# Kernel tuning notes

Measured on AMD Instinct MI355X. Metric: run time of the kernel, lower is better.

Reference implementation:

```python
import jax, jax.numpy as jnp
import numpy as np

B, C, H, W = 16, 256, 64, 64
K, HID, ITERS, EPS = 4, 512, 3, 1e-8


def _ln(x, g, b, eps=1e-5):
    m = jnp.mean(x, axis=-1, keepdims=True)
    v = jnp.mean((x - m) ** 2, axis=-1, keepdims=True)
    return (x - m) * jax.lax.rsqrt(v + eps) * g + b


def setup_inputs() -> dict:
    key = jax.random.key(0)
    ks = jax.random.split(key, 24)

    def lin(k, o, i):
        lim = np.sqrt(6.0 / (o + i)).astype(np.float32)
        return jax.random.uniform(k, (o, i), jnp.float32, -lim, lim)

    return {
        "x": jax.random.normal(ks[0], (B, C, H, W), jnp.float32),
        "noise": jax.random.normal(ks[1], (B, K, C), jnp.float32),
        "slot_mu": jax.random.normal(ks[2], (1, 1, C), jnp.float32),
        "slot_log_sigma": jnp.zeros((1, 1, C), jnp.float32),
        "ln_in_g": jnp.ones((C,)), "ln_in_b": jnp.zeros((C,)),
        "ln_sl_g": jnp.ones((C,)), "ln_sl_b": jnp.zeros((C,)),
        "ln_mlp_g": jnp.ones((C,)), "ln_mlp_b": jnp.zeros((C,)),
        "Wq": lin(ks[3], C, C), "bq": jnp.zeros((C,)),
        "Wk": lin(ks[4], C, C), "bk": jnp.zeros((C,)),
        "Wv": lin(ks[5], C, C), "bv": jnp.zeros((C,)),
        "Wu": lin(ks[6], C, 2 * C), "bu": jnp.zeros((C,)),
        "W1": lin(ks[7], HID, C), "b1": jnp.zeros((HID,)),
        "W2": lin(ks[8], C, HID), "b2": jnp.zeros((C,)),
        "We1": lin(ks[9], C // 2, C), "be1": jnp.zeros((C // 2,)),
        "We2": lin(ks[10], 1, C // 2), "be2": jnp.zeros((1,)),
    }


def reference(x, noise, slot_mu, slot_log_sigma, ln_in_g, ln_in_b, ln_sl_g, ln_sl_b,
              ln_mlp_g, ln_mlp_b, Wq, bq, Wk, bk, Wv, bv, Wu, bu, W1, b1, W2, b2,
              We1, be1, We2, be2):
    # b c h w -> b (h w) c
    xn = x.reshape(B, C, H * W).transpose(0, 2, 1)
    xn = _ln(xn, ln_in_g, ln_in_b)
    # k, v depend only on xn; hoisted out of the loop (same math)
    k = jnp.einsum('bnc,dc->bnd', xn, Wk) + bk
    v = jnp.einsum('bnc,dc->bnd', xn, Wv) + bv
    scale = C ** (-0.5)
    slots = slot_mu + jnp.exp(slot_log_sigma) * noise
    for _ in range(ITERS):
        prev = slots
        s = _ln(slots, ln_sl_g, ln_sl_b)
        q = jnp.einsum('bkc,dc->bkd', s, Wq) + bq
        attn = jax.nn.softmax(jnp.einsum('bkc,bnc->bkn', q, k) * scale, axis=1)
        w = attn / (jnp.sum(attn, axis=-1, keepdims=True) + EPS)
        updates = jnp.einsum('bkn,bnc->bkc', w, v)
        combined = jnp.concatenate([prev, updates], axis=-1)  # (B,K,2C)
        slots = jnp.einsum('bkc,dc->bkd', combined, Wu) + bu + prev
        m = _ln(slots, ln_mlp_g, ln_mlp_b)
        h = jax.nn.gelu(jnp.einsum('bkc,hc->bkh', m, W1) + b1, approximate=False)
        slots = slots + jnp.einsum('bkh,ch->bkc', h, W2) + b2
    e = jax.nn.gelu(jnp.einsum('bkc,dc->bkd', slots, We1) + be1, approximate=False)
    slot_weights = jax.nn.sigmoid(jnp.einsum('bkd,od->bko', e, We2) + be2)[..., 0]
    return slots, slot_weights
```

## Files before the change

kernel.cpp:

```cpp
#include <hip/hip_runtime.h>
#include <math.h>

#define B_    16
#define C_    256
#define NPIX  4096
#define K_    4
#define HID_  512
#define ITERS_ 3
#define NROWS (B_*NPIX)

typedef __attribute__((ext_vector_type(8))) short bf16x8;
typedef __attribute__((ext_vector_type(4))) float f32x4;

__device__ __forceinline__ float gelu_f(float x) {
    return 0.5f * x * (1.0f + erff(x * 0.70710678118654752f));
}

__device__ __forceinline__ unsigned short f2bf(float x) {
    union { float f; unsigned u; } v; v.f = x;
    unsigned r = v.u + 0x7fffu + ((v.u >> 16) & 1u);
    return (unsigned short)(r >> 16);
}
__device__ __forceinline__ float bflo(unsigned u) {
    union { unsigned u; float f; } v; v.u = u << 16; return v.f;
}
__device__ __forceinline__ float bfhi(unsigned u) {
    union { unsigned u; float f; } v; v.u = u & 0xffff0000u; return v.f;
}
__device__ __forceinline__ float4 shfl_xor4(float4 v, int m) {
    v.x = __shfl_xor(v.x, m); v.y = __shfl_xor(v.y, m);
    v.z = __shfl_xor(v.z, m); v.w = __shfl_xor(v.w, m);
    return v;
}

__device__ __forceinline__ void async_load16(const void* g, void* l) {
    __builtin_amdgcn_global_load_lds(
        (const __attribute__((address_space(1))) unsigned int*)g,
        (__attribute__((address_space(3))) unsigned int*)l, 16, 0, 0);
}

__device__ __forceinline__ void block_reduce2(float v1, float v2, float* red1, float* red2,
                                              int tid, float& o1, float& o2) {
    red1[tid] = v1; red2[tid] = v2;
    __syncthreads();
    for (int s = 128; s > 0; s >>= 1) {
        if (tid < s) { red1[tid] += red1[tid + s]; red2[tid] += red2[tid + s]; }
        __syncthreads();
    }
    o1 = red1[0]; o2 = red2[0];
    __syncthreads();
}

__global__ void prep_kernel(const float* __restrict__ Wk, const float* __restrict__ Wv,
                            const float* __restrict__ Wq, const float* __restrict__ Wu,
                            const float* __restrict__ W1, const float* __restrict__ W2,
                            const float* __restrict__ We1,
                            unsigned short* __restrict__ Wtb, float* __restrict__ WqT,
                            float* __restrict__ WuT, float* __restrict__ W1T,
                            float* __restrict__ W2T, float* __restrict__ We1T) {
    int t = blockIdx.x * 256 + threadIdx.x;
    if (t < 131072) {
        int d = t >> 8, c = t & 255;
        float v = (d < 256) ? Wk[d * 256 + c] : Wv[(d - 256) * 256 + c];
        Wtb[t] = f2bf(v);
    } else if (t < 196608) {
        int i = t - 131072; int c = i >> 8, d = i & 255;
        WqT[i] = Wq[d * 256 + c];
    } else if (t < 327680) {
        int i = t - 196608; int c = i >> 8, d = i & 255;
        WuT[i] = Wu[d * 512 + c];
    } else if (t < 458752) {
        int i = t - 327680; int c = i >> 9, h = i & 511;
        W1T[i] = W1[h * 256 + c];
    } else if (t < 589824) {
        int i = t - 458752; int h = i >> 8, d = i & 255;
        W2T[i] = W2[d * 512 + h];
    } else if (t < 622592) {
        int i = t - 589824; int c = i >> 7, e = i & 127;
        We1T[i] = We1[e * 256 + c];
    }
}

__global__ __launch_bounds__(256) void xn_fused_kernel(
    const float* __restrict__ x, const float* __restrict__ g, const float* __restrict__ bta,
    unsigned short* __restrict__ xnb) {
    __shared__ float tile[256][65];
    __shared__ float sg[256], sb[256];
    __shared__ float red1[256], red2[256];
    __shared__ float smean[64], srstd[64];
    const int tid = threadIdx.x;
    const int nt = blockIdx.x << 6, b = blockIdx.y;

    sg[tid] = g[tid]; sb[tid] = bta[tid];
    #pragma unroll
    for (int r = 0; r < 64; ++r) {
        int idx = tid + (r << 8);
        int c_l = idx >> 6, n_l = idx & 63;
        tile[c_l][n_l] = x[(size_t)(b * C_ + c_l) * NPIX + nt + n_l];
    }
    __syncthreads();
    {
        int cq = tid >> 6, n_l = tid & 63;
        float s = 0.f, s2 = 0.f;
        #pragma unroll 8
        for (int c = cq * 64; c < cq * 64 + 64; ++c) {
            float v = tile[c][n_l];
            s += v; s2 += v * v;
        }
        red1[tid] = s; red2[tid] = s2;
    }
    __syncthreads();
    if (tid < 64) {
        float s  = red1[tid] + red1[tid + 64] + red1[tid + 128] + red1[tid + 192];
        float s2 = red2[tid] + red2[tid + 64] + red2[tid + 128] + red2[tid + 192];
        float m = s * (1.0f / C_);
        smean[tid] = m;
        srstd[tid] = rsqrtf(s2 * (1.0f / C_) - m * m + 1e-5f);
    }
    __syncthreads();
    #pragma unroll
    for (int r = 0; r < 32; ++r) {
        int idx = tid + (r << 8);
        int n_l = idx >> 7, cp = idx & 127;
        int c0 = cp << 1;
        float mn = smean[n_l], rs = srstd[n_l];
        float v0 = (tile[c0][n_l] - mn) * rs * sg[c0] + sb[c0];
        float v1 = (tile[c0 + 1][n_l] - mn) * rs * sg[c0 + 1] + sb[c0 + 1];
        ushort2 o; o.x = f2bf(v0); o.y = f2bf(v1);
        *reinterpret_cast<ushort2*>(&xnb[((size_t)(b * NPIX + nt + n_l)) * C_ + c0]) = o;
    }
}

__global__ __launch_bounds__(256) void kv_gemm_mfma(
    const unsigned short* __restrict__ xnb, const unsigned short* __restrict__ Wtb,
    const float* __restrict__ bk, const float* __restrict__ bv,
    unsigned short* __restrict__ kbuf, unsigned short* __restrict__ vbuf) {
    __shared__ __align__(16) short As[128 * 32];
    __shared__ __align__(16) short Bs[128 * 32];
    const int tid = threadIdx.x;
    const int wave = tid >> 6, lane = tid & 63;
    const int mtile = blockIdx.x << 7;
    const int ntile = blockIdx.y << 7;
    const int wr = wave >> 1, wc = wave & 1;

    f32x4 acc[4][4];
    #pragma unroll
    for (int i = 0; i < 4; ++i)
        #pragma unroll
        for (int j = 0; j < 4; ++j) acc[i][j] = (f32x4)0.f;

    const int lrow = lane >> 2;
    const int lk   = (lane & 3) << 3;

    for (int kc0 = 0; kc0 < C_; kc0 += 32) {
        #pragma unroll
        for (int j = 0; j < 2; ++j) {
            int row = (wave << 5) + (j << 4) + lrow;
            async_load16(&xnb[(size_t)(mtile + row) * C_ + kc0 + lk],
                         &As[(wave << 10) + (j << 9)]);
            async_load16(&Wtb[(size_t)(ntile + row) * C_ + kc0 + lk],
                         &Bs[(wave << 10) + (j << 9)]);
        }
        __syncthreads();
        bf16x8 af[4], bfr[4];
        #pragma unroll
        for (int mi = 0; mi < 4; ++mi)
            af[mi] = *reinterpret_cast<const bf16x8*>(
                &As[((wr << 6) + (mi << 4) + (lane & 15)) * 32 + ((lane >> 4) << 3)]);
        #pragma unroll
        for (int ni = 0; ni < 4; ++ni)
            bfr[ni] = *reinterpret_cast<const bf16x8*>(
                &Bs[((wc << 6) + (ni << 4) + (lane & 15)) * 32 + ((lane >> 4) << 3)]);
        #pragma unroll
        for (int mi = 0; mi < 4; ++mi)
            #pragma unroll
            for (int ni = 0; ni < 4; ++ni)
                acc[mi][ni] = __builtin_amdgcn_mfma_f32_16x16x32_bf16(
                    af[mi], bfr[ni], acc[mi][ni], 0, 0, 0);
        __syncthreads();
    }

    #pragma unroll
    for (int ni = 0; ni < 4; ++ni) {
        int col = ntile + (wc << 6) + (ni << 4) + (lane & 15);
        bool is_k = (col < 256);
        float bias = is_k ? bk[col] : bv[col - 256];
        unsigned short* obuf = is_k ? kbuf : vbuf;
        int cl = is_k ? col : (col - 256);
        #pragma unroll
        for (int mi = 0; mi < 4; ++mi) {
            int row0 = mtile + (wr << 6) + (mi << 4) + ((lane >> 4) << 2);
            #pragma unroll
            for (int r = 0; r < 4; ++r)
                obuf[(size_t)(row0 + r) * C_ + cl] = f2bf(acc[mi][ni][r] + bias);
        }
    }
}

__device__ __forceinline__ void ln_q_body(float v, int tid, int r,
                                          const float* __restrict__ g_sl,
                                          const float* __restrict__ b_sl,
                                          const float* __restrict__ WqT,
                                          const float* __restrict__ bq,
                                          float* __restrict__ qbuf,
                                          float* snorm, float* red1, float* red2) {
    float sm, s2;
    block_reduce2(v, v * v, red1, red2, tid, sm, s2);
    float m = sm * (1.f / C_);
    float rs = rsqrtf(s2 * (1.f / C_) - m * m + 1e-5f);
    snorm[tid] = (v - m) * rs * g_sl[tid] + b_sl[tid];
    __syncthreads();
    float q0 = 0.f, q1 = 0.f, q2 = 0.f, q3 = 0.f;
    #pragma unroll 8
    for (int c = 0; c < C_; c += 4) {
        q0 = fmaf(WqT[(c + 0) * C_ + tid], snorm[c + 0], q0);
        q1 = fmaf(WqT[(c + 1) * C_ + tid], snorm[c + 1], q1);
        q2 = fmaf(WqT[(c + 2) * C_ + tid], snorm[c + 2], q2);
        q3 = fmaf(WqT[(c + 3) * C_ + tid], snorm[c + 3], q3);
    }
    qbuf[r * C_ + tid] = (q0 + q1) + (q2 + q3) + bq[tid];
}

__global__ __launch_bounds__(256) void slot_init_q_kernel(
    const float* __restrict__ noise, const float* __restrict__ mu,
    const float* __restrict__ log_sigma,
    const float* __restrict__ g_sl, const float* __restrict__ b_sl,
    const float* __restrict__ WqT, const float* __restrict__ bq,
    float* __restrict__ slots, float* __restrict__ qbuf) {
    __shared__ float snorm[256];
    __shared__ float red1[256], red2[256];
    int tid = threadIdx.x;
    int r = blockIdx.x;
    float v = mu[tid] + expf(log_sigma[tid]) * noise[r * C_ + tid];
    slots[r * C_ + tid] = v;
    ln_q_body(v, tid, r, g_sl, b_sl, WqT, bq, qbuf, snorm, red1, red2);
}

__global__ __launch_bounds__(256) void attn_fused_kernel(
    const float* __restrict__ qbuf, const unsigned short* __restrict__ kbuf,
    const unsigned short* __restrict__ vbuf,
    float* __restrict__ partials, float* __restrict__ asump) {
    __shared__ float4 qT[264];
    __shared__ float attns[K_][64];
    __shared__ float upd_s[K_][256];
    __shared__ float asw[4][4];

    const int tid = threadIdx.x;
    const int b = blockIdx.y;
    const int chunk = blockIdx.x;
    const int n0 = chunk << 6;
    const int wave = tid >> 6, lane = tid & 63;

    {
        int c = tid;
        float4 qv;
        qv.x = qbuf[b * 1024 + c];
        qv.y = qbuf[b * 1024 + 256 + c];
        qv.z = qbuf[b * 1024 + 512 + c];
        qv.w = qbuf[b * 1024 + 768 + c];
        qT[c + (c >> 5)] = qv;
    }
    __syncthreads();

    const int cpart = tid & 7;
    const int npair = tid >> 3;
    const int c0 = cpart << 5;
    float4 acc0 = {0.f, 0.f, 0.f, 0.f}, acc1 = {0.f, 0.f, 0.f, 0.f};
    const unsigned short* kbase = kbuf + ((size_t)b * NPIX + n0 + npair * 2) * C_ + c0;
    #pragma unroll
    for (int j = 0; j < 4; ++j) {
        uint4 k0 = *reinterpret_cast<const uint4*>(kbase + j * 8);
        uint4 k1 = *reinterpret_cast<const uint4*>(kbase + C_ + j * 8);
        const unsigned kw0[4] = {k0.x, k0.y, k0.z, k0.w};
        const unsigned kw1[4] = {k1.x, k1.y, k1.z, k1.w};
        #pragma unroll
        for (int jj = 0; jj < 4; ++jj) {
            int cidx = c0 + j * 8 + jj * 2 + cpart;
            float4 qa = qT[cidx];
            float4 qb = qT[cidx + 1];
            float f00 = bflo(kw0[jj]), f01 = bfhi(kw0[jj]);
            float f10 = bflo(kw1[jj]), f11 = bfhi(kw1[jj]);
            acc0.x += f00 * qa.x + f01 * qb.x;  acc0.y += f00 * qa.y + f01 * qb.y;
            acc0.z += f00 * qa.z + f01 * qb.z;  acc0.w += f00 * qa.w + f01 * qb.w;
            acc1.x += f10 * qa.x + f11 * qb.x;  acc1.y += f10 * qa.y + f11 * qb.y;
            acc1.z += f10 * qa.z + f11 * qb.z;  acc1.w += f10 * qa.w + f11 * qb.w;
        }
    }
    #pragma unroll
    for (int m = 1; m <= 4; m <<= 1) {
        acc0 = acc0 + shfl_xor4(acc0, m);
        acc1 = acc1 + shfl_xor4(acc1, m);
    }
    float4 w0, w1;
    {
        float4 l = acc0 * 0.0625f;
        float mx = fmaxf(fmaxf(l.x, l.y), fmaxf(l.z, l.w));
        w0.x = expf(l.x - mx); w0.y = expf(l.y - mx);
        w0.z = expf(l.z - mx); w0.w = expf(l.w - mx);
        float inv = 1.0f / (w0.x + w0.y + w0.z + w0.w);
        w0 = w0 * inv;
        l = acc1 * 0.0625f;
        mx = fmaxf(fmaxf(l.x, l.y), fmaxf(l.z, l.w));
        w1.x = expf(l.x - mx); w1.y = expf(l.y - mx);
        w1.z = expf(l.z - mx); w1.w = expf(l.w - mx);
        inv = 1.0f / (w1.x + w1.y + w1.z + w1.w);
        w1 = w1 * inv;
    }
    if (cpart == 0) {
        int n_l = npair * 2;
        attns[0][n_l] = w0.x; attns[1][n_l] = w0.y; attns[2][n_l] = w0.z; attns[3][n_l] = w0.w;
        attns[0][n_l + 1] = w1.x; attns[1][n_l + 1] = w1.y;
        attns[2][n_l + 1] = w1.z; attns[3][n_l + 1] = w1.w;
    }
    float4 ws = w0 + w1;
    #pragma unroll
    for (int m = 8; m <= 32; m <<= 1) ws = ws + shfl_xor4(ws, m);
    if (lane == 0) {
        asw[wave][0] = ws.x; asw[wave][1] = ws.y; asw[wave][2] = ws.z; asw[wave][3] = ws.w;
    }
    __syncthreads();
    if (tid < 4)
        asump[(b * 64 + chunk) * 4 + tid] =
            asw[0][tid] + asw[1][tid] + asw[2][tid] + asw[3][tid];

    const int h = wave >> 1;
    const int chalf = (wave & 1) << 7;
    const int c = chalf + lane * 2;
    float a0[K_] = {0.f, 0.f, 0.f, 0.f};
    float a1[K_] = {0.f, 0.f, 0.f, 0.f};
    const unsigned short* vbase = vbuf + ((size_t)b * NPIX + n0 + h * 32) * C_ + c;
    #pragma unroll 4
    for (int nn = 0; nn < 32; ++nn) {
        unsigned vv = *reinterpret_cast<const unsigned*>(vbase + (size_t)nn * C_);
        float v0 = bflo(vv), v1 = bfhi(vv);
        int n_l = h * 32 + nn;
        float q0 = attns[0][n_l], q1 = attns[1][n_l], q2 = attns[2][n_l], q3 = attns[3][n_l];
        a0[0] = fmaf(q0, v0, a0[0]); a1[0] = fmaf(q0, v1, a1[0]);
        a0[1] = fmaf(q1, v0, a0[1]); a1[1] = fmaf(q1, v1, a1[1]);
        a0[2] = fmaf(q2, v0, a0[2]); a1[2] = fmaf(q2, v1, a1[2]);
        a0[3] = fmaf(q3, v0, a0[3]); a1[3] = fmaf(q3, v1, a1[3]);
    }
    __syncthreads();
    if (h == 0) {
        #pragma unroll
        for (int k = 0; k < K_; ++k) { upd_s[k][c] = a0[k]; upd_s[k][c + 1] = a1[k]; }
    }
    __syncthreads();
    if (h == 1) {
        #pragma unroll
        for (int k = 0; k < K_; ++k) { upd_s[k][c] += a0[k]; upd_s[k][c + 1] += a1[k]; }
    }
    __syncthreads();
    float* pb = partials + (size_t)(b * 64 + chunk) * (K_ * 256);
    #pragma unroll
    for (int k = 0; k < K_; ++k) pb[k * 256 + tid] = upd_s[k][tid];
}

__device__ __forceinline__ float slot_update_body(
    int tid, int r, const float* __restrict__ slots,
    const float* __restrict__ partials, const float* __restrict__ asump,
    const float* __restrict__ WuT, const float* __restrict__ bu,
    const float* __restrict__ g_mlp, const float* __restrict__ b_mlp,
    const float* __restrict__ W1T, const float* __restrict__ b1,
    const float* __restrict__ W2T, const float* __restrict__ b2,
    float* comb, float* mrow, float* hrow, float* red1, float* red2) {
    int b = r >> 2, kk = r & 3;
    float prev = slots[r * C_ + tid];
    comb[tid] = prev;
    float u0 = 0.f, u1 = 0.f;
    #pragma unroll 8
    for (int j = 0; j < 64; j += 2) {
        u0 += partials[((size_t)(b * 64 + j) * 4 + kk) * 256 + tid];
        u1 += partials[((size_t)(b * 64 + j + 1) * 4 + kk) * 256 + tid];
    }
    float dv = (tid < 64) ? asump[(b * 64 + tid) * 4 + kk] : 0.f;
    float sm_d, dummy;
    block_reduce2(dv, 0.f, red1, red2, tid, sm_d, dummy);
    comb[256 + tid] = (u0 + u1) / (sm_d + 1e-8f);
    __syncthreads();
    float n0 = 0.f, n1 = 0.f, n2 = 0.f, n3 = 0.f;
    #pragma unroll 8
    for (int c = 0; c < 512; c += 4) {
        n0 = fmaf(WuT[(c + 0) * C_ + tid], comb[c + 0], n0);
        n1 = fmaf(WuT[(c + 1) * C_ + tid], comb[c + 1], n1);
        n2 = fmaf(WuT[(c + 2) * C_ + tid], comb[c + 2], n2);
        n3 = fmaf(WuT[(c + 3) * C_ + tid], comb[c + 3], n3);
    }
    float nv = (n0 + n1) + (n2 + n3) + bu[tid] + prev;
    float sm, s2;
    block_reduce2(nv, nv * nv, red1, red2, tid, sm, s2);
    float m = sm * (1.f / C_);
    float rs = rsqrtf(s2 * (1.f / C_) - m * m + 1e-5f);
    mrow[tid] = (nv - m) * rs * g_mlp[tid] + b_mlp[tid];
    __syncthreads();
    #pragma unroll
    for (int rep = 0; rep < 2; ++rep) {
        int j = tid + rep * 256;
        float h0 = 0.f, h1 = 0.f, h2 = 0.f, h3 = 0.f;
        #pragma unroll 8
        for (int c = 0; c < C_; c += 4) {
            h0 = fmaf(W1T[(c + 0) * HID_ + j], mrow[c + 0], h0);
            h1 = fmaf(W1T[(c + 1) * HID_ + j], mrow[c + 1], h1);
            h2 = fmaf(W1T[(c + 2) * HID_ + j], mrow[c + 2], h2);
            h3 = fmaf(W1T[(c + 3) * HID_ + j], mrow[c + 3], h3);
        }
        hrow[j] = gelu_f((h0 + h1) + (h2 + h3) + b1[j]);
    }
    __syncthreads();
    float o0 = 0.f, o1 = 0.f, o2 = 0.f, o3 = 0.f;
    #pragma unroll 8
    for (int h = 0; h < 512; h += 4) {
        o0 = fmaf(W2T[(h + 0) * C_ + tid], hrow[h + 0], o0);
        o1 = fmaf(W2T[(h + 1) * C_ + tid], hrow[h + 1], o1);
        o2 = fmaf(W2T[(h + 2) * C_ + tid], hrow[h + 2], o2);
        o3 = fmaf(W2T[(h + 3) * C_ + tid], hrow[h + 3], o3);
    }
    return nv + (o0 + o1) + (o2 + o3) + b2[tid];
}

__global__ __launch_bounds__(256) void slot_update_q_kernel(
    float* __restrict__ slots, const float* __restrict__ partials, const float* __restrict__ asump,
    const float* __restrict__ WuT, const float* __restrict__ bu,
    const float* __restrict__ g_mlp, const float* __restrict__ b_mlp,
    const float* __restrict__ W1T, const float* __restrict__ b1,
    const float* __restrict__ W2T, const float* __restrict__ b2,
    const float* __restrict__ g_sl, const float* __restrict__ b_sl,
    const float* __restrict__ WqT, const float* __restrict__ bq,
    float* __restrict__ qbuf) {
    __shared__ float comb[512];
    __shared__ float mrow[256];
    __shared__ float hrow[512];
    __shared__ float red1[256], red2[256];
    int tid = threadIdx.x;
    int r = blockIdx.x;
    float ov = slot_update_body(tid, r, slots, partials, asump, WuT, bu, g_mlp, b_mlp,
                                W1T, b1, W2T, b2, comb, mrow, hrow, red1, red2);
    slots[r * C_ + tid] = ov;
    __syncthreads();
    ln_q_body(ov, tid, r, g_sl, b_sl, WqT, bq, qbuf, mrow, red1, red2);
}

__global__ __launch_bounds__(256) void slot_update_final_kernel(
    float* __restrict__ slots, const float* __restrict__ partials, const float* __restrict__ asump,
    const float* __restrict__ WuT, const float* __restrict__ bu,
    const float* __restrict__ g_mlp, const float* __restrict__ b_mlp,
    const float* __restrict__ W1T, const float* __restrict__ b1,
    const float* __restrict__ W2T, const float* __restrict__ b2,
    const float* __restrict__ We1T, const float* __restrict__ be1,
    const float* __restrict__ We2, const float* __restrict__ be2,
    float* __restrict__ out) {
    __shared__ float comb[512];
    __shared__ float mrow[256];
    __shared__ float hrow[512];
    __shared__ float red1[256], red2[256];
    __shared__ float erow[128];
    int tid = threadIdx.x;
    int r = blockIdx.x;
    float ov = slot_update_body(tid, r, slots, partials, asump, WuT, bu, g_mlp, b_mlp,
                                W1T, b1, W2T, b2, comb, mrow, hrow, red1, red2);
    out[r * C_ + tid] = ov;
    mrow[tid] = ov;
    __syncthreads();
    if (tid < 128) {
        float e0 = 0.f, e1 = 0.f, e2 = 0.f, e3 = 0.f;
        #pragma unroll 8
        for (int c = 0; c < C_; c += 4) {
            e0 = fmaf(We1T[(c + 0) * 128 + tid], mrow[c + 0], e0);
            e1 = fmaf(We1T[(c + 1) * 128 + tid], mrow[c + 1], e1);
            e2 = fmaf(We1T[(c + 2) * 128 + tid], mrow[c + 2], e2);
            e3 = fmaf(We1T[(c + 3) * 128 + tid], mrow[c + 3], e3);
        }
        erow[tid] = gelu_f((e0 + e1) + (e2 + e3) + be1[tid]);
    }
    __syncthreads();
    if (tid == 0) {
        float acc = be2[0];
        #pragma unroll 8
        for (int j = 0; j < 128; ++j) acc = fmaf(We2[j], erow[j], acc);
        out[B_ * K_ * C_ + r] = 1.0f / (1.0f + expf(-acc));
    }
}

extern "C" void kernel_launch(void* const* d_in, const int* in_sizes, int n_in,
                              void* d_out, int out_size, void* d_ws, size_t ws_size,
                              hipStream_t stream) {
    (void)in_sizes; (void)n_in; (void)out_size; (void)ws_size;
    const float* x        = (const float*)d_in[0];
    const float* noise    = (const float*)d_in[1];
    const float* slot_mu  = (const float*)d_in[2];
    const float* slot_ls  = (const float*)d_in[3];
    const float* ln_in_g  = (const float*)d_in[4];
    const float* ln_in_b  = (const float*)d_in[5];
    const float* ln_sl_g  = (const float*)d_in[6];
    const float* ln_sl_b  = (const float*)d_in[7];
    const float* ln_mlp_g = (const float*)d_in[8];
    const float* ln_mlp_b = (const float*)d_in[9];
    const float* Wq = (const float*)d_in[10];
    const float* bq = (const float*)d_in[11];
    const float* Wk = (const float*)d_in[12];
    const float* bk = (const float*)d_in[13];
    const float* Wv = (const float*)d_in[14];
    const float* bv = (const float*)d_in[15];
    const float* Wu = (const float*)d_in[16];
    const float* bu = (const float*)d_in[17];
    const float* W1 = (const float*)d_in[18];
    const float* b1 = (const float*)d_in[19];
    const float* W2 = (const float*)d_in[20];
    const float* b2 = (const float*)d_in[21];
    const float* We1 = (const float*)d_in[22];
    const float* be1 = (const float*)d_in[23];
    const float* We2 = (const float*)d_in[24];
    const float* be2 = (const float*)d_in[25];
    float* out = (float*)d_out;

    char* ws = (char*)d_ws;
    unsigned short* kbuf = (unsigned short*)ws;
    unsigned short* vbuf = kbuf + (size_t)NROWS * C_;
    unsigned short* xnb  = vbuf + (size_t)NROWS * C_;
    unsigned short* Wtb  = xnb + (size_t)NROWS * C_;
    float* WqT  = (float*)(Wtb + 512 * C_);
    float* WuT  = WqT + 256 * 256;
    float* W1T  = WuT + 512 * 256;
    float* W2T  = W1T + 256 * 512;
    float* We1T = W2T + 512 * 256;
    float* slots = We1T + 256 * 128;
    float* qbuf  = slots + B_ * K_ * C_;
    float* partials = qbuf + B_ * K_ * C_;
    float* asump = partials + (size_t)B_ * 64 * K_ * 256;

    prep_kernel<<<2432, 256, 0, stream>>>(Wk, Wv, Wq, Wu, W1, W2, We1,
                                          Wtb, WqT, WuT, W1T, W2T, We1T);
    xn_fused_kernel<<<dim3(64, 16), 256, 0, stream>>>(x, ln_in_g, ln_in_b, xnb);
    slot_init_q_kernel<<<B_ * K_, 256, 0, stream>>>(noise, slot_mu, slot_ls,
                                                    ln_sl_g, ln_sl_b, WqT, bq, slots, qbuf);
    kv_gemm_mfma<<<dim3(512, 4), 256, 0, stream>>>(xnb, Wtb, bk, bv, kbuf, vbuf);
    for (int it = 0; it < ITERS_; ++it) {
        attn_fused_kernel<<<dim3(64, 16), 256, 0, stream>>>(qbuf, kbuf, vbuf, partials, asump);
        if (it < ITERS_ - 1) {
            slot_update_q_kernel<<<B_ * K_, 256, 0, stream>>>(
                slots, partials, asump, WuT, bu, ln_mlp_g, ln_mlp_b, W1T, b1, W2T, b2,
                ln_sl_g, ln_sl_b, WqT, bq, qbuf);
        } else {
            slot_update_final_kernel<<<B_ * K_, 256, 0, stream>>>(
                slots, partials, asump, WuT, bu, ln_mlp_g, ln_mlp_b, W1T, b1, W2T, b2,
                We1T, be1, We2, be2, out);
        }
    }
}
```

Before: 371.3 us.

## Use float4-packed weight layouts for slot MLPs and stage KV GEMM output through LDS

The weight transposes in prep are replaced with a float4-interleaved layout, so the per-slot matvecs (q, update, MLP, head) each issue one 16-byte load and use LDS vector reads. The KV GEMM loads A/B tiles in MFMA fragment order, removing index arithmetic on LDS reads. It also writes its results to an LDS tile first and then stores 16-byte rows, replacing scattered 2-byte global stores. The partial-sum reduction uses more accumulators, and the extra LDS tile (about 34 KB) may lower GEMM occupancy.

```diff
diff --git a/kernel.cpp b/kernel.cpp
--- a/kernel.cpp
+++ b/kernel.cpp
@@ -32,6 +32,13 @@
     v.z = __shfl_xor(v.z, m); v.w = __shfl_xor(v.w, m);
     return v;
 }
+__device__ __forceinline__ void fma4(float4& a, const float4 w, const float4 s) {
+    a.x = fmaf(w.x, s.x, a.x); a.y = fmaf(w.y, s.y, a.y);
+    a.z = fmaf(w.z, s.z, a.z); a.w = fmaf(w.w, s.w, a.w);
+}
+__device__ __forceinline__ float hsum4(const float4 a) {
+    return (a.x + a.y) + (a.z + a.w);
+}
 
 __device__ __forceinline__ void async_load16(const void* g, void* l) {
     __builtin_amdgcn_global_load_lds(
@@ -55,29 +62,32 @@
                             const float* __restrict__ Wq, const float* __restrict__ Wu,
                             const float* __restrict__ W1, const float* __restrict__ W2,
                             const float* __restrict__ We1,
-                            unsigned short* __restrict__ Wtb, float* __restrict__ WqT,
-                            float* __restrict__ WuT, float* __restrict__ W1T,
-                            float* __restrict__ W2T, float* __restrict__ We1T) {
+                            unsigned short* __restrict__ Wtb, float4* __restrict__ Wq4,
+                            float4* __restrict__ Wu4, float4* __restrict__ W14,
+                            float4* __restrict__ W24, float4* __restrict__ We14) {
     int t = blockIdx.x * 256 + threadIdx.x;
     if (t < 131072) {
         int d = t >> 8, c = t & 255;
         float v = (d < 256) ? Wk[d * 256 + c] : Wv[(d - 256) * 256 + c];
         Wtb[t] = f2bf(v);
-    } else if (t < 196608) {
-        int i = t - 131072; int c = i >> 8, d = i & 255;
-        WqT[i] = Wq[d * 256 + c];
-    } else if (t < 327680) {
-        int i = t - 196608; int c = i >> 8, d = i & 255;
-        WuT[i] = Wu[d * 512 + c];
-    } else if (t < 458752) {
-        int i = t - 327680; int c = i >> 9, h = i & 511;
-        W1T[i] = W1[h * 256 + c];
-    } else if (t < 589824) {
-        int i = t - 458752; int h = i >> 8, d = i & 255;
-        W2T[i] = W2[d * 512 + h];
-    } else if (t < 622592) {
-        int i = t - 589824; int c = i >> 7, e = i & 127;
-        We1T[i] = We1[e * 256 + c];
+    } else {
+        int i = t - 131072;
+        if (i < 16384) {
+            int c4 = i >> 8, d = i & 255;
+            Wq4[i] = *(const float4*)&Wq[d * 256 + c4 * 4];
+        } else if (i < 49152) {
+            int i2 = i - 16384; int c4 = i2 >> 8, d = i2 & 255;
+            Wu4[i2] = *(const float4*)&Wu[d * 512 + c4 * 4];
+        } else if (i < 81920) {
+            int i2 = i - 49152; int c4 = i2 >> 9, h = i2 & 511;
+            W14[i2] = *(const float4*)&W1[h * 256 + c4 * 4];
+        } else if (i < 114688) {
+            int i2 = i - 81920; int h4 = i2 >> 8, d = i2 & 255;
+            W24[i2] = *(const float4*)&W2[d * 512 + h4 * 4];
+        } else {
+            int i2 = i - 114688; int c4 = i2 >> 7, e = i2 & 127;
+            We14[i2] = *(const float4*)&We1[e * 256 + c4 * 4];
+        }
     }
 }
 
@@ -137,6 +147,7 @@
     unsigned short* __restrict__ kbuf, unsigned short* __restrict__ vbuf) {
     __shared__ __align__(16) short As[128 * 32];
     __shared__ __align__(16) short Bs[128 * 32];
+    __shared__ __align__(16) unsigned short Cs[128 * 136];
     const int tid = threadIdx.x;
     const int wave = tid >> 6, lane = tid & 63;
     const int mtile = blockIdx.x << 7;
@@ -149,28 +160,25 @@
         #pragma unroll
         for (int j = 0; j < 4; ++j) acc[i][j] = (f32x4)0.f;
 
-    const int lrow = lane >> 2;
-    const int lk   = (lane & 3) << 3;
+    const int lrow = lane & 15;
+    const int lk   = (lane >> 4) << 3;
 
     for (int kc0 = 0; kc0 < C_; kc0 += 32) {
         #pragma unroll
         for (int j = 0; j < 2; ++j) {
-            int row = (wave << 5) + (j << 4) + lrow;
-            async_load16(&xnb[(size_t)(mtile + row) * C_ + kc0 + lk],
-                         &As[(wave << 10) + (j << 9)]);
-            async_load16(&Wtb[(size_t)(ntile + row) * C_ + kc0 + lk],
-                         &Bs[(wave << 10) + (j << 9)]);
+            int st = (wave << 1) + j;
+            int row = (st << 4) + lrow;
+            async_load16(&xnb[(size_t)(mtile + row) * C_ + kc0 + lk], &As[st << 9]);
+            async_load16(&Wtb[(size_t)(ntile + row) * C_ + kc0 + lk], &Bs[st << 9]);
         }
         __syncthreads();
         bf16x8 af[4], bfr[4];
         #pragma unroll
         for (int mi = 0; mi < 4; ++mi)
-            af[mi] = *reinterpret_cast<const bf16x8*>(
-                &As[((wr << 6) + (mi << 4) + (lane & 15)) * 32 + ((lane >> 4) << 3)]);
+            af[mi] = *reinterpret_cast<const bf16x8*>(&As[(((wr << 2) + mi) << 9) + lane * 8]);
         #pragma unroll
         for (int ni = 0; ni < 4; ++ni)
-            bfr[ni] = *reinterpret_cast<const bf16x8*>(
-                &Bs[((wc << 6) + (ni << 4) + (lane & 15)) * 32 + ((lane >> 4) << 3)]);
+            bfr[ni] = *reinterpret_cast<const bf16x8*>(&Bs[(((wc << 2) + ni) << 9) + lane * 8]);
         #pragma unroll
         for (int mi = 0; mi < 4; ++mi)
             #pragma unroll
@@ -182,25 +190,34 @@
 
     #pragma unroll
     for (int ni = 0; ni < 4; ++ni) {
-        int col = ntile + (wc << 6) + (ni << 4) + (lane & 15);
-        bool is_k = (col < 256);
-        float bias = is_k ? bk[col] : bv[col - 256];
-        unsigned short* obuf = is_k ? kbuf : vbuf;
-        int cl = is_k ? col : (col - 256);
+        int col_l = (wc << 6) + (ni << 4) + (lane & 15);
+        int gcol = ntile + col_l;
+        float bias = (gcol < 256) ? bk[gcol] : bv[gcol - 256];
         #pragma unroll
         for (int mi = 0; mi < 4; ++mi) {
-            int row0 = mtile + (wr << 6) + (mi << 4) + ((lane >> 4) << 2);
+            int row0 = (wr << 6) + (mi << 4) + ((lane >> 4) << 2);
             #pragma unroll
             for (int r = 0; r < 4; ++r)
-                obuf[(size_t)(row0 + r) * C_ + cl] = f2bf(acc[mi][ni][r] + bias);
-        }
+                Cs[(row0 + r) * 136 + col_l] = f2bf(acc[mi][ni][r] + bias);
+        }
+    }
+    __syncthreads();
+    unsigned short* obuf = (blockIdx.y < 2) ? kbuf : vbuf;
+    const int cb = (blockIdx.y & 1) << 7;
+    #pragma unroll
+    for (int rep = 0; rep < 8; ++rep) {
+        int idx = (rep << 8) + tid;
+        int row = idx >> 4;
+        int ch = (idx & 15) << 3;
+        uint4 d = *reinterpret_cast<const uint4*>(&Cs[row * 136 + ch]);
+        *reinterpret_cast<uint4*>(&obuf[(size_t)(mtile + row) * C_ + cb + ch]) = d;
     }
 }
 
 __device__ __forceinline__ void ln_q_body(float v, int tid, int r,
                                           const float* __restrict__ g_sl,
                                           const float* __restrict__ b_sl,
-                                          const float* __restrict__ WqT,
+                                          const float4* __restrict__ Wq4,
                                           const float* __restrict__ bq,
                                           float* __restrict__ qbuf,
                                           float* snorm, float* red1, float* red2) {
@@ -210,30 +227,33 @@
     float rs = rsqrtf(s2 * (1.f / C_) - m * m + 1e-5f);
     snorm[tid] = (v - m) * rs * g_sl[tid] + b_sl[tid];
     __syncthreads();
-    float q0 = 0.f, q1 = 0.f, q2 = 0.f, q3 = 0.f;
-    #pragma unroll 8
-    for (int c = 0; c < C_; c += 4) {
-        q0 = fmaf(WqT[(c + 0) * C_ + tid], snorm[c + 0], q0);
-        q1 = fmaf(WqT[(c + 1) * C_ + tid], snorm[c + 1], q1);
-        q2 = fmaf(WqT[(c + 2) * C_ + tid], snorm[c + 2], q2);
-        q3 = fmaf(WqT[(c + 3) * C_ + tid], snorm[c + 3], q3);
-    }
-    qbuf[r * C_ + tid] = (q0 + q1) + (q2 + q3) + bq[tid];
+    const float4* sn4 = (const float4*)snorm;
+    float4 a0 = {0,0,0,0}, a1 = {0,0,0,0}, a2 = {0,0,0,0}, a3 = {0,0,0,0};
+    #pragma unroll 4
+    for (int c4 = 0; c4 < 64; c4 += 4) {
+        float4 w0 = Wq4[(c4 + 0) * 256 + tid];
+        float4 w1 = Wq4[(c4 + 1) * 256 + tid];
+        float4 w2 = Wq4[(c4 + 2) * 256 + tid];
+        float4 w3 = Wq4[(c4 + 3) * 256 + tid];
+        fma4(a0, w0, sn4[c4 + 0]); fma4(a1, w1, sn4[c4 + 1]);
+        fma4(a2, w2, sn4[c4 + 2]); fma4(a3, w3, sn4[c4 + 3]);
+    }
+    qbuf[r * C_ + tid] = (hsum4(a0) + hsum4(a1)) + (hsum4(a2) + hsum4(a3)) + bq[tid];
 }
 
 __global__ __launch_bounds__(256) void slot_init_q_kernel(
     const float* __restrict__ noise, const float* __restrict__ mu,
     const float* __restrict__ log_sigma,
     const float* __restrict__ g_sl, const float* __restrict__ b_sl,
-    const float* __restrict__ WqT, const float* __restrict__ bq,
+    const float4* __restrict__ Wq4, const float* __restrict__ bq,
     float* __restrict__ slots, float* __restrict__ qbuf) {
-    __shared__ float snorm[256];
+    __shared__ __align__(16) float snorm[256];
     __shared__ float red1[256], red2[256];
     int tid = threadIdx.x;
     int r = blockIdx.x;
     float v = mu[tid] + expf(log_sigma[tid]) * noise[r * C_ + tid];
     slots[r * C_ + tid] = v;
-    ln_q_body(v, tid, r, g_sl, b_sl, WqT, bq, qbuf, snorm, red1, red2);
+    ln_q_body(v, tid, r, g_sl, b_sl, Wq4, bq, qbuf, snorm, red1, red2);
 }
 
 __global__ __launch_bounds__(256) void attn_fused_kernel(
@@ -359,118 +379,129 @@
 __device__ __forceinline__ float slot_update_body(
     int tid, int r, const float* __restrict__ slots,
     const float* __restrict__ partials, const float* __restrict__ asump,
-    const float* __restrict__ WuT, const float* __restrict__ bu,
+    const float4* __restrict__ Wu4, const float* __restrict__ bu,
     const float* __restrict__ g_mlp, const float* __restrict__ b_mlp,
-    const float* __restrict__ W1T, const float* __restrict__ b1,
-    const float* __restrict__ W2T, const float* __restrict__ b2,
+    const float4* __restrict__ W14, const float* __restrict__ b1,
+    const float4* __restrict__ W24, const float* __restrict__ b2,
     float* comb, float* mrow, float* hrow, float* red1, float* red2) {
     int b = r >> 2, kk = r & 3;
     float prev = slots[r * C_ + tid];
     comb[tid] = prev;
-    float u0 = 0.f, u1 = 0.f;
-    #pragma unroll 8
-    for (int j = 0; j < 64; j += 2) {
-        u0 += partials[((size_t)(b * 64 + j) * 4 + kk) * 256 + tid];
-        u1 += partials[((size_t)(b * 64 + j + 1) * 4 + kk) * 256 + tid];
-    }
+    const float* pbase = partials + (size_t)b * 65536 + kk * 256 + tid;
+    float u0 = 0.f, u1 = 0.f, u2 = 0.f, u3 = 0.f, u4 = 0.f, u5 = 0.f, u6 = 0.f, u7 = 0.f;
+    #pragma unroll
+    for (int j = 0; j < 64; j += 8) {
+        u0 += pbase[(j + 0) * 1024]; u1 += pbase[(j + 1) * 1024];
+        u2 += pbase[(j + 2) * 1024]; u3 += pbase[(j + 3) * 1024];
+        u4 += pbase[(j + 4) * 1024]; u5 += pbase[(j + 5) * 1024];
+        u6 += pbase[(j + 6) * 1024]; u7 += pbase[(j + 7) * 1024];
+    }
+    float usum = ((u0 + u1) + (u2 + u3)) + ((u4 + u5) + (u6 + u7));
     float dv = (tid < 64) ? asump[(b * 64 + tid) * 4 + kk] : 0.f;
     float sm_d, dummy;
     block_reduce2(dv, 0.f, red1, red2, tid, sm_d, dummy);
-    comb[256 + tid] = (u0 + u1) / (sm_d + 1e-8f);
-    __syncthreads();
-    float n0 = 0.f, n1 = 0.f, n2 = 0.f, n3 = 0.f;
-    #pragma unroll 8
-    for (int c = 0; c < 512; c += 4) {
-        n0 = fmaf(WuT[(c + 0) * C_ + tid], comb[c + 0], n0);
-        n1 = fmaf(WuT[(c + 1) * C_ + tid], comb[c + 1], n1);
-        n2 = fmaf(WuT[(c + 2) * C_ + tid], comb[c + 2], n2);
-        n3 = fmaf(WuT[(c + 3) * C_ + tid], comb[c + 3], n3);
-    }
-    float nv = (n0 + n1) + (n2 + n3) + bu[tid] + prev;
+    comb[256 + tid] = usum / (sm_d + 1e-8f);
+    __syncthreads();
+    const float4* cb4 = (const float4*)comb;
+    float4 a0 = {0,0,0,0}, a1 = {0,0,0,0}, a2 = {0,0,0,0}, a3 = {0,0,0,0};
+    #pragma unroll 4
+    for (int c4 = 0; c4 < 128; c4 += 4) {
+        float4 w0 = Wu4[(c4 + 0) * 256 + tid];
+        float4 w1 = Wu4[(c4 + 1) * 256 + tid];
+        float4 w2 = Wu4[(c4 + 2) * 256 + tid];
+        float4 w3 = Wu4[(c4 + 3) * 256 + tid];
+        fma4(a0, w0, cb4[c4 + 0]); fma4(a1, w1, cb4[c4 + 1]);
+        fma4(a2, w2, cb4[c4 + 2]); fma4(a3, w3, cb4[c4 + 3]);
+    }
+    float nv = (hsum4(a0) + hsum4(a1)) + (hsum4(a2) + hsum4(a3)) + bu[tid] + prev;
     float sm, s2;
     block_reduce2(nv, nv * nv, red1, red2, tid, sm, s2);
     float m = sm * (1.f / C_);
     float rs = rsqrtf(s2 * (1.f / C_) - m * m + 1e-5f);
     mrow[tid] = (nv - m) * rs * g_mlp[tid] + b_mlp[tid];
     __syncthreads();
-    #pragma unroll
-    for (int rep = 0; rep < 2; ++rep) {
-        int j = tid + rep * 256;
-        float h0 = 0.f, h1 = 0.f, h2 = 0.f, h3 = 0.f;
-        #pragma unroll 8
-        for (int c = 0; c < C_; c += 4) {
-            h0 = fmaf(W1T[(c + 0) * HID_ + j], mrow[c + 0], h0);
-            h1 = fmaf(W1T[(c + 1) * HID_ + j], mrow[c + 1], h1);
-            h2 = fmaf(W1T[(c + 2) * HID_ + j], mrow[c + 2], h2);
-            h3 = fmaf(W1T[(c + 3) * HID_ + j], mrow[c + 3], h3);
-        }
-        hrow[j] = gelu_f((h0 + h1) + (h2 + h3) + b1[j]);
-    }
-    __syncthreads();
-    float o0 = 0.f, o1 = 0.f, o2 = 0.f, o3 = 0.f;
-    #pragma unroll 8
-    for (int h = 0; h < 512; h += 4) {
-        o0 = fmaf(W2T[(h + 0) * C_ + tid], hrow[h + 0], o0);
-        o1 = fmaf(W2T[(h + 1) * C_ + tid], hrow[h + 1], o1);
-        o2 = fmaf(W2T[(h + 2) * C_ + tid], hrow[h + 2], o2);
-        o3 = fmaf(W2T[(h + 3) * C_ + tid], hrow[h + 3], o3);
-    }
-    return nv + (o0 + o1) + (o2 + o3) + b2[tid];
+    const float4* m4 = (const float4*)mrow;
+    float4 p0 = {0,0,0,0}, p1 = {0,0,0,0}, p2 = {0,0,0,0}, p3 = {0,0,0,0};
+    #pragma unroll 4
+    for (int c4 = 0; c4 < 64; c4 += 2) {
+        float4 wa0 = W14[(c4 + 0) * 512 + tid];
+        float4 wb0 = W14[(c4 + 0) * 512 + tid + 256];
+        float4 wa1 = W14[(c4 + 1) * 512 + tid];
+        float4 wb1 = W14[(c4 + 1) * 512 + tid + 256];
+        float4 s0 = m4[c4 + 0], s1 = m4[c4 + 1];
+        fma4(p0, wa0, s0); fma4(p1, wa1, s1);
+        fma4(p2, wb0, s0); fma4(p3, wb1, s1);
+    }
+    hrow[tid]       = gelu_f(hsum4(p0) + hsum4(p1) + b1[tid]);
+    hrow[tid + 256] = gelu_f(hsum4(p2) + hsum4(p3) + b1[tid + 256]);
+    __syncthreads();
+    const float4* h4 = (const float4*)hrow;
+    float4 o0 = {0,0,0,0}, o1 = {0,0,0,0}, o2 = {0,0,0,0}, o3 = {0,0,0,0};
+    #pragma unroll 4
+    for (int q4 = 0; q4 < 128; q4 += 4) {
+        float4 w0 = W24[(q4 + 0) * 256 + tid];
+        float4 w1 = W24[(q4 + 1) * 256 + tid];
+        float4 w2 = W24[(q4 + 2) * 256 + tid];
+        float4 w3 = W24[(q4 + 3) * 256 + tid];
+        fma4(o0, w0, h4[q4 + 0]); fma4(o1, w1, h4[q4 + 1]);
+        fma4(o2, w2, h4[q4 + 2]); fma4(o3, w3, h4[q4 + 3]);
+    }
+    return nv + (hsum4(o0) + hsum4(o1)) + (hsum4(o2) + hsum4(o3)) + b2[tid];
 }
 
 __global__ __launch_bounds__(256) void slot_update_q_kernel(
     float* __restrict__ slots, const float* __restrict__ partials, const float* __restrict__ asump,
-    const float* __restrict__ WuT, const float* __restrict__ bu,
+    const float4* __restrict__ Wu4, const float* __restrict__ bu,
     const float* __restrict__ g_mlp, const float* __restrict__ b_mlp,
-    const float* __restrict__ W1T, const float* __restrict__ b1,
-    const float* __restrict__ W2T, const float* __restrict__ b2,
+    const float4* __restrict__ W14, const float* __restrict__ b1,
+    const float4* __restrict__ W24, const float* __restrict__ b2,
     const float* __restrict__ g_sl, const float* __restrict__ b_sl,
-    const float* __restrict__ WqT, const float* __restrict__ bq,
+    const float4* __restrict__ Wq4, const float* __restrict__ bq,
     float* __restrict__ qbuf) {
-    __shared__ float comb[512];
-    __shared__ float mrow[256];
-    __shared__ float hrow[512];
+    __shared__ __align__(16) float comb[512];
+    __shared__ __align__(16) float mrow[256];
+    __shared__ __align__(16) float hrow[512];
     __shared__ float red1[256], red2[256];
     int tid = threadIdx.x;
     int r = blockIdx.x;
-    float ov = slot_update_body(tid, r, slots, partials, asump, WuT, bu, g_mlp, b_mlp,
-                                W1T, b1, W2T, b2, comb, mrow, hrow, red1, red2);
+    float ov = slot_update_body(tid, r, slots, partials, asump, Wu4, bu, g_mlp, b_mlp,
+                                W14, b1, W24, b2, comb, mrow, hrow, red1, red2);
     slots[r * C_ + tid] = ov;
     __syncthreads();
-    ln_q_body(ov, tid, r, g_sl, b_sl, WqT, bq, qbuf, mrow, red1, red2);
+    ln_q_body(ov, tid, r, g_sl, b_sl, Wq4, bq, qbuf, mrow, red1, red2);
 }
 
 __global__ __launch_bounds__(256) void slot_update_final_kernel(
     float* __restrict__ slots, const float* __restrict__ partials, const float* __restrict__ asump,
-    const float* __restrict__ WuT, const float* __restrict__ bu,
+    const float4* __restrict__ Wu4, const float* __restrict__ bu,
     const float* __restrict__ g_mlp, const float* __restrict__ b_mlp,
-    const float* __restrict__ W1T, const float* __restrict__ b1,
-    const float* __restrict__ W2T, const float* __restrict__ b2,
-    const float* __restrict__ We1T, const float* __restrict__ be1,
+    const float4* __restrict__ W14, const float* __restrict__ b1,
+    const float4* __restrict__ W24, const float* __restrict__ b2,
+    const float4* __restrict__ We14, const float* __restrict__ be1,
     const float* __restrict__ We2, const float* __restrict__ be2,
     float* __restrict__ out) {
-    __shared__ float comb[512];
-    __shared__ float mrow[256];
-    __shared__ float hrow[512];
+    __shared__ __align__(16) float comb[512];
+    __shared__ __align__(16) float mrow[256];
+    __shared__ __align__(16) float hrow[512];
     __shared__ float red1[256], red2[256];
     __shared__ float erow[128];
     int tid = threadIdx.x;
     int r = blockIdx.x;
-    float ov = slot_update_body(tid, r, slots, partials, asump, WuT, bu, g_mlp, b_mlp,
-                                W1T, b1, W2T, b2, comb, mrow, hrow, red1, red2);
+    float ov = slot_update_body(tid, r, slots, partials, asump, Wu4, bu, g_mlp, b_mlp,
+                                W14, b1, W24, b2, comb, mrow, hrow, red1, red2);
     out[r * C_ + tid] = ov;
     mrow[tid] = ov;
     __syncthreads();
     if (tid < 128) {
-        float e0 = 0.f, e1 = 0.f, e2 = 0.f, e3 = 0.f;
-        #pragma unroll 8
-        for (int c = 0; c < C_; c += 4) {
-            e0 = fmaf(We1T[(c + 0) * 128 + tid], mrow[c + 0], e0);
-            e1 = fmaf(We1T[(c + 1) * 128 + tid], mrow[c + 1], e1);
-            e2 = fmaf(We1T[(c + 2) * 128 + tid], mrow[c + 2], e2);
-            e3 = fmaf(We1T[(c + 3) * 128 + tid], mrow[c + 3], e3);
-        }
-        erow[tid] = gelu_f((e0 + e1) + (e2 + e3) + be1[tid]);
+        const float4* m4 = (const float4*)mrow;
+        float4 e0 = {0,0,0,0}, e1 = {0,0,0,0};
+        #pragma unroll 4
+        for (int c4 = 0; c4 < 64; c4 += 2) {
+            float4 w0 = We14[(c4 + 0) * 128 + tid];
+            float4 w1 = We14[(c4 + 1) * 128 + tid];
+            fma4(e0, w0, m4[c4 + 0]); fma4(e1, w1, m4[c4 + 1]);
+        }
+        erow[tid] = gelu_f(hsum4(e0) + hsum4(e1) + be1[tid]);
     }
     __syncthreads();
     if (tid == 0) {
@@ -518,32 +549,32 @@
     unsigned short* vbuf = kbuf + (size_t)NROWS * C_;
     unsigned short* xnb  = vbuf + (size_t)NROWS * C_;
     unsigned short* Wtb  = xnb + (size_t)NROWS * C_;
-    float* WqT  = (float*)(Wtb + 512 * C_);
-    float* WuT  = WqT + 256 * 256;
-    float* W1T  = WuT + 512 * 256;
-    float* W2T  = W1T + 256 * 512;
-    float* We1T = W2T + 512 * 256;
-    float* slots = We1T + 256 * 128;
+    float4* Wq4  = (float4*)(Wtb + 512 * C_);
+    float4* Wu4  = Wq4 + 16384;
+    float4* W14  = Wu4 + 32768;
+    float4* W24  = W14 + 32768;
+    float4* We14 = W24 + 32768;
+    float* slots = (float*)(We14 + 8192);
     float* qbuf  = slots + B_ * K_ * C_;
     float* partials = qbuf + B_ * K_ * C_;
     float* asump = partials + (size_t)B_ * 64 * K_ * 256;
 
-    prep_kernel<<<2432, 256, 0, stream>>>(Wk, Wv, Wq, Wu, W1, W2, We1,
-                                          Wtb, WqT, WuT, W1T, W2T, We1T);
+    prep_kernel<<<992, 256, 0, stream>>>(Wk, Wv, Wq, Wu, W1, W2, We1,
+                                         Wtb, Wq4, Wu4, W14, W24, We14);
     xn_fused_kernel<<<dim3(64, 16), 256, 0, stream>>>(x, ln_in_g, ln_in_b, xnb);
     slot_init_q_kernel<<<B_ * K_, 256, 0, stream>>>(noise, slot_mu, slot_ls,
-                                                    ln_sl_g, ln_sl_b, WqT, bq, slots, qbuf);
+                                                    ln_sl_g, ln_sl_b, Wq4, bq, slots, qbuf);
     kv_gemm_mfma<<<dim3(512, 4), 256, 0, stream>>>(xnb, Wtb, bk, bv, kbuf, vbuf);
     for (int it = 0; it < ITERS_; ++it) {
         attn_fused_kernel<<<dim3(64, 16), 256, 0, stream>>>(qbuf, kbuf, vbuf, partials, asump);
         if (it < ITERS_ - 1) {
             slot_update_q_kernel<<<B_ * K_, 256, 0, stream>>>(
-                slots, partials, asump, WuT, bu, ln_mlp_g, ln_mlp_b, W1T, b1, W2T, b2,
-                ln_sl_g, ln_sl_b, WqT, bq, qbuf);
+                slots, partials, asump, Wu4, bu, ln_mlp_g, ln_mlp_b, W14, b1, W24, b2,
+                ln_sl_g, ln_sl_b, Wq4, bq, qbuf);
         } else {
             slot_update_final_kernel<<<B_ * K_, 256, 0, stream>>>(
-                slots, partials, asump, WuT, bu, ln_mlp_g, ln_mlp_b, W1T, b1, W2T, b2,
-                We1T, be1, We2, be2, out);
-        }
-    }
-}
+                slots, partials, asump, Wu4, bu, ln_mlp_g, ln_mlp_b, W14, b1, W24, b2,
+                We14, be1, We2, be2, out);
+        }
+    }
+}
```

Measured after the change: 400.8 us. 8.0% more time.
